# Kernel optimization log

Measured on AMD Instinct MI355X. Metric: run time of the kernel, lower is better.

The kernel has to match this reference:

```python
import jax, jax.numpy as jnp
import numpy as np

D_MODEL = 2048
N_HEADS = 16
D_K = D_MODEL // N_HEADS
D_FF = 5504
THETA = 10000.0
EPS = 1e-5


def rmsnorm(x, g):
    xf = x.astype(jnp.float32)
    ms = jnp.mean(xf * xf, axis=-1, keepdims=True)
    return (xf / jnp.sqrt(ms + EPS) * g).astype(x.dtype)


def rope_tables(seq_len):
    k = jnp.arange(D_K // 2, dtype=jnp.float32)
    freqs = THETA ** (-2.0 * k / float(D_K))          # [d_k/2]
    pos = jnp.arange(seq_len, dtype=jnp.float32)
    phases = pos[:, None] * freqs[None, :]            # [S, d_k/2]
    return jnp.cos(phases), jnp.sin(phases)


def apply_rope(x, cos, sin):
    # x: [..., S, d_k]; cos/sin: [S, d_k/2]
    x_even = x[..., 0::2]
    x_odd = x[..., 1::2]
    e = x_even * cos - x_odd * sin
    o = x_even * sin + x_odd * cos
    out = jnp.stack([e, o], axis=-1)                  # [..., S, d_k/2, 2]
    return out.reshape(x.shape)


def setup_inputs() -> dict:
    key = jax.random.key(0)
    ks = jax.random.split(key, 9)
    def tn(k, shape, fan_in, fan_out):
        std = np.sqrt(2.0 / (fan_in + fan_out))
        return (jax.random.truncated_normal(k, -3.0, 3.0, shape, jnp.float32) * std)
    B, S = 2, 2048
    return {
        "x": jax.random.normal(ks[0], (B, S, D_MODEL), jnp.float32),
        "Wq": tn(ks[1], (D_MODEL, D_MODEL), D_MODEL, D_MODEL),
        "Wk": tn(ks[2], (D_MODEL, D_MODEL), D_MODEL, D_MODEL),
        "Wv": tn(ks[3], (D_MODEL, D_MODEL), D_MODEL, D_MODEL),
        "Wo": tn(ks[4], (D_MODEL, D_MODEL), D_MODEL, D_MODEL),
        "W1": tn(ks[5], (D_FF, D_MODEL), D_MODEL, D_FF),
        "W2": tn(ks[6], (D_MODEL, D_FF), D_FF, D_MODEL),
        "W3": tn(ks[7], (D_FF, D_MODEL), D_MODEL, D_FF),
        "g1": jnp.ones((D_MODEL,), jnp.float32),
        "g2": jnp.ones((D_MODEL,), jnp.float32),
    }


def reference(x, Wq, Wk, Wv, Wo, W1, W2, W3, g1, g2):
    B, S, D = x.shape
    # --- attention sublayer (pre-norm) ---
    xn = rmsnorm(x, g1)
    q = jnp.einsum('bsd,ed->bse', xn, Wq).reshape(B, S, N_HEADS, D_K).transpose(0, 2, 1, 3)
    k = jnp.einsum('bsd,ed->bse', xn, Wk).reshape(B, S, N_HEADS, D_K).transpose(0, 2, 1, 3)
    v = jnp.einsum('bsd,ed->bse', xn, Wv).reshape(B, S, N_HEADS, D_K).transpose(0, 2, 1, 3)
    cos, sin = rope_tables(S)
    q = apply_rope(q, cos, sin)
    k = apply_rope(k, cos, sin)
    scores = jnp.einsum('bhqd,bhkd->bhqk', q, k) / jnp.sqrt(jnp.float32(D_K))
    causal = jnp.tril(jnp.ones((S, S), bool))         # True = keep
    scores = jnp.where(causal, scores, -jnp.inf)
    attn = jax.nn.softmax(scores, axis=-1)
    out = jnp.einsum('bhqk,bhkd->bhqd', attn, v)
    out = out.transpose(0, 2, 1, 3).reshape(B, S, D)
    out = jnp.einsum('bse,de->bsd', out, Wo)
    x_res = x + out
    # --- SwiGLU FFN sublayer (pre-norm) ---
    xn2 = rmsnorm(x_res, g2)
    w1x = jnp.einsum('bsd,fd->bsf', xn2, W1)
    w3x = jnp.einsum('bsd,fd->bsf', xn2, W3)
    h = (w1x * jax.nn.sigmoid(w1x)) * w3x
    ff = jnp.einsum('bsf,df->bsd', h, W2)
    return x_res + ff
```

## Files before the change

### kernel.cpp

```cpp
#include <hip/hip_runtime.h>
#include <hip/hip_bf16.h>
#include <math.h>


typedef __bf16 bf16x8 __attribute__((ext_vector_type(8)));
typedef float f32x4 __attribute__((ext_vector_type(4)));

#define MFMA16(a, b, c) __builtin_amdgcn_mfma_f32_16x16x32_bf16(a, b, c, 0, 0, 0)

__device__ __forceinline__ void async_cp16(const void* g, void* l) {
  __builtin_amdgcn_global_load_lds((__attribute__((address_space(1))) void*)g,
                                   (__attribute__((address_space(3))) void*)l,
                                   16, 0, 0);
}

__global__ __launch_bounds__(256) void cvt_k(const float* __restrict__ s,
                                             __bf16* __restrict__ d, long n) {
  const long i = ((long)blockIdx.x * 256 + threadIdx.x) * 8;
  if (i >= n) return;
  f32x4 a = *(const f32x4*)(s + i);
  f32x4 b = *(const f32x4*)(s + i + 4);
  bf16x8 o;
#pragma unroll
  for (int j = 0; j < 4; ++j) {
    o[j] = (__bf16)a[j];
    o[4 + j] = (__bf16)b[j];
  }
  *(bf16x8*)(d + i) = o;
}

template <int EPI, typename CT, typename RT>
__global__ __launch_bounds__(256) void gemm_bt(
    const __bf16* __restrict__ A, const __bf16* __restrict__ B,
    CT* C, const RT* R, int M, int N, int K) {
  __shared__ __attribute__((aligned(16))) __bf16 sA[128 * 32];
  __shared__ __attribute__((aligned(16))) __bf16 sB[128 * 32];
  const int tid = threadIdx.x;
  const int lane = tid & 63;
  const int wave = tid >> 6;
  const int wm = (wave >> 1) << 6;
  const int wn = (wave & 1) << 6;
  const int ln15 = lane & 15;
  const int kq8 = (lane >> 4) << 3;
  const long blockM = (long)blockIdx.y << 7;
  const long blockN = (long)blockIdx.x << 7;

  const int srow = tid >> 2;
  const int scol = (tid & 3) << 3;
  const __bf16* gA = A + (blockM + srow) * (long)K + scol;
  const __bf16* gB = B + (blockN + srow) * (long)K + scol;
  __bf16* lA = sA + tid * 8;
  __bf16* lB = sB + tid * 8;

  f32x4 acc[4][4] = {};
  const int KT = K >> 5;

  async_cp16(gA, lA);
  async_cp16(gA + 64 * (long)K, lA + 2048);
  async_cp16(gB, lB);
  async_cp16(gB + 64 * (long)K, lB + 2048);

  for (int kt = 0; kt < KT; ++kt) {
    __builtin_amdgcn_s_waitcnt(0);
    __syncthreads();
    bf16x8 af[4], bfr[4];
#pragma unroll
    for (int i = 0; i < 4; ++i)
      af[i] = *(const bf16x8*)&sA[(wm + i * 16 + ln15) * 32 + kq8];
#pragma unroll
    for (int j = 0; j < 4; ++j)
      bfr[j] = *(const bf16x8*)&sB[(wn + j * 16 + ln15) * 32 + kq8];
    __syncthreads();
    if (kt + 1 < KT) {
      const __bf16* a2 = gA + (long)(kt + 1) * 32;
      const __bf16* b2 = gB + (long)(kt + 1) * 32;
      async_cp16(a2, lA);
      async_cp16(a2 + 64 * (long)K, lA + 2048);
      async_cp16(b2, lB);
      async_cp16(b2 + 64 * (long)K, lB + 2048);
    }
#pragma unroll
    for (int i = 0; i < 4; ++i)
#pragma unroll
      for (int j = 0; j < 4; ++j)
        acc[i][j] = MFMA16(af[i], bfr[j], acc[i][j]);
  }

  const int rq4 = (lane >> 4) << 2;
#pragma unroll
  for (int i = 0; i < 4; ++i)
#pragma unroll
    for (int j = 0; j < 4; ++j)
#pragma unroll
      for (int r = 0; r < 4; ++r) {
        const long grow = blockM + wm + i * 16 + rq4 + r;
        const long gcol = blockN + wn + j * 16 + ln15;
        const long idx = grow * N + gcol;
        float v = acc[i][j][r];
        if (EPI == 1) v += (float)R[idx];
        if (EPI == 2) {
          const float w = (float)R[idx];
          v *= w / (1.f + __expf(-w));
        }
        C[idx] = (CT)v;
      }
}

__global__ __launch_bounds__(64) void attn_k(
    const __bf16* __restrict__ q, const __bf16* __restrict__ k,
    const __bf16* __restrict__ v, __bf16* __restrict__ o) {
  __shared__ __attribute__((aligned(16))) __bf16 sP[16 * 32];
  const int lane = threadIdx.x;
  const int ln15 = lane & 15;
  const int quad = lane >> 4;
  const int qt = blockIdx.x;
  const int h = blockIdx.y;
  const int b = blockIdx.z;
  const int S = 2048;
  const int qb = qt << 4;
  const long bh = (long)b * S * 2048 + h * 128;
  const float NEG = -1.0e4f;

  bf16x8 qf[4];
  const __bf16* qp = q + bh + (long)(qb + ln15) * 2048 + quad * 8;
#pragma unroll
  for (int kb = 0; kb < 4; ++kb) qf[kb] = *(const bf16x8*)(qp + kb * 32);

  f32x4 oacc[8] = {};
  float mrow[4] = {NEG, NEG, NEG, NEG};
  float lrow[4] = {};
  const float scale = 0.08838834764831845f;

  const int nkt = (qt + 2) >> 1;
  for (int kt = 0; kt < nkt; ++kt) {
    const int kbase = kt << 5;
    f32x4 s[2] = {};
#pragma unroll
    for (int c = 0; c < 2; ++c) {
      const __bf16* kp = k + bh + (long)(kbase + c * 16 + ln15) * 2048 + quad * 8;
#pragma unroll
      for (int kb = 0; kb < 4; ++kb) {
        bf16x8 kf = *(const bf16x8*)(kp + kb * 32);
        s[c] = MFMA16(qf[kb], kf, s[c]);
      }
    }
#pragma unroll
    for (int r = 0; r < 4; ++r) {
      const int qrow = qb + quad * 4 + r;
      const bool m0 = (kbase + ln15 > qrow);
      const bool m1 = (kbase + 16 + ln15 > qrow);
      const float s0 = m0 ? NEG : s[0][r] * scale;
      const float s1 = m1 ? NEG : s[1][r] * scale;
      float tm = fmaxf(s0, s1);
#pragma unroll
      for (int off = 1; off < 16; off <<= 1) tm = fmaxf(tm, __shfl_xor(tm, off));
      const float mnew = fmaxf(mrow[r], tm);
      const float alpha = __expf(mrow[r] - mnew);
      mrow[r] = mnew;
      const float p0 = m0 ? 0.f : __expf(s0 - mnew);
      const float p1 = m1 ? 0.f : __expf(s1 - mnew);
      float rs = p0 + p1;
#pragma unroll
      for (int off = 1; off < 16; off <<= 1) rs += __shfl_xor(rs, off);
      lrow[r] = lrow[r] * alpha + rs;
#pragma unroll
      for (int nt = 0; nt < 8; ++nt) oacc[nt][r] *= alpha;
      sP[(quad * 4 + r) * 32 + ln15] = (__bf16)p0;
      sP[(quad * 4 + r) * 32 + 16 + ln15] = (__bf16)p1;
    }
    __syncthreads();
    bf16x8 pa = *(const bf16x8*)&sP[ln15 * 32 + quad * 8];
    __syncthreads();
    const __bf16* vbase = v + bh + (long)kbase * 2048;
#pragma unroll
    for (int nt = 0; nt < 8; ++nt) {
      bf16x8 vf;
      const __bf16* vp = vbase + (long)(quad * 8) * 2048 + nt * 16 + ln15;
#pragma unroll
      for (int j = 0; j < 8; ++j) vf[j] = vp[(long)j * 2048];
      oacc[nt] = MFMA16(pa, vf, oacc[nt]);
    }
  }

  __bf16* op = o + bh + (long)qb * 2048;
#pragma unroll
  for (int nt = 0; nt < 8; ++nt)
#pragma unroll
    for (int r = 0; r < 4; ++r)
      op[(long)(quad * 4 + r) * 2048 + nt * 16 + ln15] =
          (__bf16)(oacc[nt][r] / lrow[r]);
}

__global__ __launch_bounds__(256) void rmsnorm_k(
    const float* __restrict__ x, const float* __restrict__ g,
    __bf16* __restrict__ out) {
  __shared__ float red[4];
  const int row = blockIdx.x;
  const int tid = threadIdx.x;
  f32x4 xa = *(const f32x4*)(x + (long)row * 2048 + tid * 8);
  f32x4 xb = *(const f32x4*)(x + (long)row * 2048 + tid * 8 + 4);
  float xf[8];
  float ss = 0.f;
#pragma unroll
  for (int j = 0; j < 4; ++j) {
    xf[j] = xa[j];
    xf[4 + j] = xb[j];
  }
#pragma unroll
  for (int j = 0; j < 8; ++j) ss += xf[j] * xf[j];
#pragma unroll
  for (int off = 32; off > 0; off >>= 1) ss += __shfl_xor(ss, off);
  if ((tid & 63) == 0) red[tid >> 6] = ss;
  __syncthreads();
  const float inv = rsqrtf((red[0] + red[1] + red[2] + red[3]) * (1.f / 2048.f) + 1e-5f);
  f32x4 ga = *(const f32x4*)(g + tid * 8);
  f32x4 gb = *(const f32x4*)(g + tid * 8 + 4);
  bf16x8 ov;
#pragma unroll
  for (int j = 0; j < 4; ++j) {
    ov[j] = (__bf16)(xf[j] * inv * ga[j]);
    ov[4 + j] = (__bf16)(xf[4 + j] * inv * gb[j]);
  }
  *(bf16x8*)(out + (long)row * 2048 + tid * 8) = ov;
}

__global__ __launch_bounds__(256) void rope_k(__bf16* __restrict__ t) {
  const long idx = (long)blockIdx.x * 256 + threadIdx.x;
  const int kp = idx & 63;
  const int h = (idx >> 6) & 15;
  const long row = idx >> 10;
  const int pos = (int)(row & 2047);
  const float freq = exp2f((float)kp * (-13.287712379549449f / 64.0f));
  float sn, cs;
  sincosf((float)pos * freq, &sn, &cs);
  __bf16* p = t + row * 2048 + h * 128 + kp * 2;
  const float e = (float)p[0], od = (float)p[1];
  p[0] = (__bf16)(e * cs - od * sn);
  p[1] = (__bf16)(e * sn + od * cs);
}

extern "C" void kernel_launch(void* const* d_in, const int* in_sizes, int n_in,
                              void* d_out, int out_size, void* d_ws, size_t ws_size,
                              hipStream_t stream) {
  const float* x = (const float*)d_in[0];
  const float* Wq = (const float*)d_in[1];
  const float* Wk = (const float*)d_in[2];
  const float* Wv = (const float*)d_in[3];
  const float* Wo = (const float*)d_in[4];
  const float* W1 = (const float*)d_in[5];
  const float* W2 = (const float*)d_in[6];
  const float* W3 = (const float*)d_in[7];
  const float* g1 = (const float*)d_in[8];
  const float* g2 = (const float*)d_in[9];
  float* out = (float*)d_out;
  char* ws = (char*)d_ws;

  const long NDD = 2048L * 2048;
  const long NFD = 5504L * 2048;
  const long WSLOT = 22544384;
  const long MB16 = 16777216;

  __bf16* wslot = (__bf16*)(ws);
  __bf16* xn = (__bf16*)(ws + WSLOT);
  __bf16* qb = (__bf16*)(ws + WSLOT + MB16);
  __bf16* kb = (__bf16*)(ws + WSLOT + 2 * MB16);
  __bf16* vb = (__bf16*)(ws + WSLOT + 3 * MB16);
  __bf16* attn = xn;
  __bf16* xn2 = vb;
  __bf16* w1x = xn;

  rmsnorm_k<<<4096, 256, 0, stream>>>(x, g1, xn);

  cvt_k<<<2048, 256, 0, stream>>>(Wq, wslot, NDD);
  gemm_bt<0, __bf16, float><<<dim3(16, 32), 256, 0, stream>>>(
      xn, wslot, qb, nullptr, 4096, 2048, 2048);
  cvt_k<<<2048, 256, 0, stream>>>(Wk, wslot, NDD);
  gemm_bt<0, __bf16, float><<<dim3(16, 32), 256, 0, stream>>>(
      xn, wslot, kb, nullptr, 4096, 2048, 2048);
  cvt_k<<<2048, 256, 0, stream>>>(Wv, wslot, NDD);
  gemm_bt<0, __bf16, float><<<dim3(16, 32), 256, 0, stream>>>(
      xn, wslot, vb, nullptr, 4096, 2048, 2048);

  rope_k<<<16384, 256, 0, stream>>>(qb);
  rope_k<<<16384, 256, 0, stream>>>(kb);
  attn_k<<<dim3(128, 16, 2), 64, 0, stream>>>(qb, kb, vb, attn);

  cvt_k<<<2048, 256, 0, stream>>>(Wo, wslot, NDD);
  gemm_bt<1, float, float><<<dim3(16, 32), 256, 0, stream>>>(
      attn, wslot, out, x, 4096, 2048, 2048);

  rmsnorm_k<<<4096, 256, 0, stream>>>(out, g2, xn2);

  cvt_k<<<5504, 256, 0, stream>>>(W1, wslot, NFD);
  gemm_bt<0, __bf16, float><<<dim3(43, 32), 256, 0, stream>>>(
      xn2, wslot, w1x, nullptr, 4096, 5504, 2048);
  cvt_k<<<5504, 256, 0, stream>>>(W3, wslot, NFD);
  gemm_bt<2, __bf16, __bf16><<<dim3(43, 32), 256, 0, stream>>>(
      xn2, wslot, w1x, w1x, 4096, 5504, 2048);
  cvt_k<<<5504, 256, 0, stream>>>(W2, wslot, NFD);
  gemm_bt<1, float, float><<<dim3(16, 32), 256, 0, stream>>>(
      w1x, wslot, out, out, 4096, 2048, 5504);
}
```

Measured before the change: 1.130 ms.

## Pre-transpose V for vectorized attention loads and schedule longest query tiles first

Adds a transpose kernel that writes V as [b, channel, seq] into the weight scratch slot. This lets the attention kernel load each MFMA B-fragment with a single 16-byte vector load instead of eight strided scalar 2-byte loads. It also reverses the query-tile order so the causally longest blocks launch first, which should balance the tail. The cost is one extra kernel and an 8 MB round trip through memory for V.

Result: slower. 1.281 ms (+13.4%).

```diff
diff --git a/kernel.cpp b/kernel.cpp
--- a/kernel.cpp
+++ b/kernel.cpp
@@ -106,19 +106,39 @@
       }
 }
 
+__global__ __launch_bounds__(256) void vt_k(const __bf16* __restrict__ v,
+                                            __bf16* __restrict__ vt) {
+  __shared__ __bf16 sT[64 * 40];
+  const int t = threadIdx.x;
+  const int s0 = blockIdx.x << 5;
+  const int c0 = blockIdx.y << 6;
+  const long b = blockIdx.z;
+  const int sl = t >> 3;
+  const int cg = (t & 7) << 3;
+  bf16x8 val = *(const bf16x8*)(v + (b * 2048 + s0 + sl) * 2048L + c0 + cg);
+#pragma unroll
+  for (int j = 0; j < 8; ++j) sT[(cg + j) * 40 + sl] = val[j];
+  __syncthreads();
+  const int cl = t >> 2;
+  const int sg = (t & 3) << 3;
+  bf16x8 o = *(const bf16x8*)&sT[cl * 40 + sg];
+  *(bf16x8*)(vt + (b * 2048 + c0 + cl) * 2048L + s0 + sg) = o;
+}
+
 __global__ __launch_bounds__(64) void attn_k(
     const __bf16* __restrict__ q, const __bf16* __restrict__ k,
-    const __bf16* __restrict__ v, __bf16* __restrict__ o) {
+    const __bf16* __restrict__ vt, __bf16* __restrict__ o) {
   __shared__ __attribute__((aligned(16))) __bf16 sP[16 * 32];
   const int lane = threadIdx.x;
   const int ln15 = lane & 15;
   const int quad = lane >> 4;
-  const int qt = blockIdx.x;
+  const int qt = (int)gridDim.x - 1 - (int)blockIdx.x;
   const int h = blockIdx.y;
   const int b = blockIdx.z;
   const int S = 2048;
   const int qb = qt << 4;
   const long bh = (long)b * S * 2048 + h * 128;
+  const __bf16* vtp = vt + ((long)b * 2048 + h * 128) * 2048;
   const float NEG = -1.0e4f;
 
   bf16x8 qf[4];
@@ -171,13 +191,10 @@
     __syncthreads();
     bf16x8 pa = *(const bf16x8*)&sP[ln15 * 32 + quad * 8];
     __syncthreads();
-    const __bf16* vbase = v + bh + (long)kbase * 2048;
 #pragma unroll
     for (int nt = 0; nt < 8; ++nt) {
-      bf16x8 vf;
-      const __bf16* vp = vbase + (long)(quad * 8) * 2048 + nt * 16 + ln15;
-#pragma unroll
-      for (int j = 0; j < 8; ++j) vf[j] = vp[(long)j * 2048];
+      bf16x8 vf = *(const bf16x8*)(vtp + (long)(nt * 16 + ln15) * 2048 +
+                                   kbase + quad * 8);
       oacc[nt] = MFMA16(pa, vf, oacc[nt]);
     }
   }
@@ -266,6 +283,7 @@
   __bf16* kb = (__bf16*)(ws + WSLOT + 2 * MB16);
   __bf16* vb = (__bf16*)(ws + WSLOT + 3 * MB16);
   __bf16* attn = xn;
+  __bf16* vtb = wslot;
   __bf16* xn2 = vb;
   __bf16* w1x = xn;
 
@@ -281,9 +299,10 @@
   gemm_bt<0, __bf16, float><<<dim3(16, 32), 256, 0, stream>>>(
       xn, wslot, vb, nullptr, 4096, 2048, 2048);
 
+  vt_k<<<dim3(64, 32, 2), 256, 0, stream>>>(vb, vtb);
   rope_k<<<16384, 256, 0, stream>>>(qb);
   rope_k<<<16384, 256, 0, stream>>>(kb);
-  attn_k<<<dim3(128, 16, 2), 64, 0, stream>>>(qb, kb, vb, attn);
+  attn_k<<<dim3(128, 16, 2), 64, 0, stream>>>(qb, kb, vtb, attn);
 
   cvt_k<<<2048, 256, 0, stream>>>(Wo, wslot, NDD);
   gemm_bt<1, float, float><<<dim3(16, 32), 256, 0, stream>>>(
```

## Pair complementary causal query tiles per attention block and remap blocks to XCDs

Applied to the files above, without the earlier changes.

Each attention workgroup now handles two 16-row query tiles, p and 127-p, so the causal work per block is balanced. K and V fragments loaded from global memory are shared by both tiles' MFMAs, which halves K/V traffic per query row. Blocks are remapped so each XCD handles contiguous (batch, head) panels, which should improve L2 locality. In exchange, register pressure rises (two sets of accumulators, with launch bounds set to 2 waves) and the grid drops to half as many blocks.

Result: faster. 1.028 ms (-9.0%).

```diff
diff --git a/kernel.cpp b/kernel.cpp
--- a/kernel.cpp
+++ b/kernel.cpp
@@ -106,89 +106,149 @@
       }
 }
 
-__global__ __launch_bounds__(64) void attn_k(
+__device__ __forceinline__ void sm_update(const f32x4 s[2], float mrow[4],
+                                          float lrow[4], f32x4 oacc[8],
+                                          __bf16* sP, int qb, int kbase,
+                                          int ln15, int quad) {
+  const float scale = 0.08838834764831845f;
+  const float NEG = -1.0e4f;
+#pragma unroll
+  for (int r = 0; r < 4; ++r) {
+    const int qrow = qb + quad * 4 + r;
+    const bool m0 = (kbase + ln15 > qrow);
+    const bool m1 = (kbase + 16 + ln15 > qrow);
+    const float s0 = m0 ? NEG : s[0][r] * scale;
+    const float s1 = m1 ? NEG : s[1][r] * scale;
+    float tm = fmaxf(s0, s1);
+#pragma unroll
+    for (int off = 1; off < 16; off <<= 1) tm = fmaxf(tm, __shfl_xor(tm, off));
+    const float mnew = fmaxf(mrow[r], tm);
+    const float alpha = __expf(mrow[r] - mnew);
+    mrow[r] = mnew;
+    const float p0 = m0 ? 0.f : __expf(s0 - mnew);
+    const float p1 = m1 ? 0.f : __expf(s1 - mnew);
+    float rs = p0 + p1;
+#pragma unroll
+    for (int off = 1; off < 16; off <<= 1) rs += __shfl_xor(rs, off);
+    lrow[r] = lrow[r] * alpha + rs;
+#pragma unroll
+    for (int nt = 0; nt < 8; ++nt) oacc[nt][r] *= alpha;
+    sP[(quad * 4 + r) * 32 + ln15] = (__bf16)p0;
+    sP[(quad * 4 + r) * 32 + 16 + ln15] = (__bf16)p1;
+  }
+}
+
+__global__ __launch_bounds__(64, 2) void attn_k(
     const __bf16* __restrict__ q, const __bf16* __restrict__ k,
     const __bf16* __restrict__ v, __bf16* __restrict__ o) {
-  __shared__ __attribute__((aligned(16))) __bf16 sP[16 * 32];
+  __shared__ __attribute__((aligned(16))) __bf16 sPA[16 * 32];
+  __shared__ __attribute__((aligned(16))) __bf16 sPB[16 * 32];
   const int lane = threadIdx.x;
   const int ln15 = lane & 15;
   const int quad = lane >> 4;
-  const int qt = blockIdx.x;
-  const int h = blockIdx.y;
-  const int b = blockIdx.z;
+  const int lin = blockIdx.x + 64 * (blockIdx.y + 16 * blockIdx.z);
+  const int xcd = lin & 7;
+  const int j = lin >> 3;
+  const int panel = xcd * 4 + (j >> 6);
+  const int p = j & 63;
+  const int b = panel >> 4;
+  const int h = panel & 15;
   const int S = 2048;
-  const int qb = qt << 4;
+  const int qbA = p << 4;
+  const int qbB = (127 - p) << 4;
   const long bh = (long)b * S * 2048 + h * 128;
+
+  bf16x8 qfA[4], qfB[4];
+  {
+    const __bf16* qpA = q + bh + (long)(qbA + ln15) * 2048 + quad * 8;
+    const __bf16* qpB = q + bh + (long)(qbB + ln15) * 2048 + quad * 8;
+#pragma unroll
+    for (int kb = 0; kb < 4; ++kb) {
+      qfA[kb] = *(const bf16x8*)(qpA + kb * 32);
+      qfB[kb] = *(const bf16x8*)(qpB + kb * 32);
+    }
+  }
+
   const float NEG = -1.0e4f;
-
-  bf16x8 qf[4];
-  const __bf16* qp = q + bh + (long)(qb + ln15) * 2048 + quad * 8;
-#pragma unroll
-  for (int kb = 0; kb < 4; ++kb) qf[kb] = *(const bf16x8*)(qp + kb * 32);
-
-  f32x4 oacc[8] = {};
-  float mrow[4] = {NEG, NEG, NEG, NEG};
-  float lrow[4] = {};
-  const float scale = 0.08838834764831845f;
-
-  const int nkt = (qt + 2) >> 1;
-  for (int kt = 0; kt < nkt; ++kt) {
+  f32x4 oaccA[8] = {}, oaccB[8] = {};
+  float mrowA[4] = {NEG, NEG, NEG, NEG}, mrowB[4] = {NEG, NEG, NEG, NEG};
+  float lrowA[4] = {}, lrowB[4] = {};
+
+  const int nktA = ((p) + 2) >> 1;
+  const int nktB = ((127 - p) + 2) >> 1;
+
+  for (int kt = 0; kt < nktB; ++kt) {
     const int kbase = kt << 5;
-    f32x4 s[2] = {};
-#pragma unroll
-    for (int c = 0; c < 2; ++c) {
-      const __bf16* kp = k + bh + (long)(kbase + c * 16 + ln15) * 2048 + quad * 8;
-#pragma unroll
-      for (int kb = 0; kb < 4; ++kb) {
-        bf16x8 kf = *(const bf16x8*)(kp + kb * 32);
-        s[c] = MFMA16(qf[kb], kf, s[c]);
-      }
-    }
+    const bool doA = (kt < nktA);
+    f32x4 sA[2] = {}, sB[2] = {};
+    if (doA) {
+#pragma unroll
+      for (int c = 0; c < 2; ++c) {
+        const __bf16* kp =
+            k + bh + (long)(kbase + c * 16 + ln15) * 2048 + quad * 8;
+#pragma unroll
+        for (int kb = 0; kb < 4; ++kb) {
+          bf16x8 kf = *(const bf16x8*)(kp + kb * 32);
+          sB[c] = MFMA16(qfB[kb], kf, sB[c]);
+          sA[c] = MFMA16(qfA[kb], kf, sA[c]);
+        }
+      }
+    } else {
+#pragma unroll
+      for (int c = 0; c < 2; ++c) {
+        const __bf16* kp =
+            k + bh + (long)(kbase + c * 16 + ln15) * 2048 + quad * 8;
+#pragma unroll
+        for (int kb = 0; kb < 4; ++kb) {
+          bf16x8 kf = *(const bf16x8*)(kp + kb * 32);
+          sB[c] = MFMA16(qfB[kb], kf, sB[c]);
+        }
+      }
+    }
+
+    sm_update(sB, mrowB, lrowB, oaccB, sPB, qbB, kbase, ln15, quad);
+    if (doA) sm_update(sA, mrowA, lrowA, oaccA, sPA, qbA, kbase, ln15, quad);
+
+    __syncthreads();
+    bf16x8 paB = *(const bf16x8*)&sPB[ln15 * 32 + quad * 8];
+    bf16x8 paA = {};
+    if (doA) paA = *(const bf16x8*)&sPA[ln15 * 32 + quad * 8];
+    __syncthreads();
+
+    const __bf16* vbase = v + bh + (long)kbase * 2048;
+    if (doA) {
+#pragma unroll
+      for (int nt = 0; nt < 8; ++nt) {
+        bf16x8 vf;
+        const __bf16* vp = vbase + (long)(quad * 8) * 2048 + nt * 16 + ln15;
+#pragma unroll
+        for (int jj = 0; jj < 8; ++jj) vf[jj] = vp[(long)jj * 2048];
+        oaccB[nt] = MFMA16(paB, vf, oaccB[nt]);
+        oaccA[nt] = MFMA16(paA, vf, oaccA[nt]);
+      }
+    } else {
+#pragma unroll
+      for (int nt = 0; nt < 8; ++nt) {
+        bf16x8 vf;
+        const __bf16* vp = vbase + (long)(quad * 8) * 2048 + nt * 16 + ln15;
+#pragma unroll
+        for (int jj = 0; jj < 8; ++jj) vf[jj] = vp[(long)jj * 2048];
+        oaccB[nt] = MFMA16(paB, vf, oaccB[nt]);
+      }
+    }
+  }
+
+  __bf16* opB = o + bh + (long)qbB * 2048;
+  __bf16* opA = o + bh + (long)qbA * 2048;
+#pragma unroll
+  for (int nt = 0; nt < 8; ++nt)
 #pragma unroll
     for (int r = 0; r < 4; ++r) {
-      const int qrow = qb + quad * 4 + r;
-      const bool m0 = (kbase + ln15 > qrow);
-      const bool m1 = (kbase + 16 + ln15 > qrow);
-      const float s0 = m0 ? NEG : s[0][r] * scale;
-      const float s1 = m1 ? NEG : s[1][r] * scale;
-      float tm = fmaxf(s0, s1);
-#pragma unroll
-      for (int off = 1; off < 16; off <<= 1) tm = fmaxf(tm, __shfl_xor(tm, off));
-      const float mnew = fmaxf(mrow[r], tm);
-      const float alpha = __expf(mrow[r] - mnew);
-      mrow[r] = mnew;
-      const float p0 = m0 ? 0.f : __expf(s0 - mnew);
-      const float p1 = m1 ? 0.f : __expf(s1 - mnew);
-      float rs = p0 + p1;
-#pragma unroll
-      for (int off = 1; off < 16; off <<= 1) rs += __shfl_xor(rs, off);
-      lrow[r] = lrow[r] * alpha + rs;
-#pragma unroll
-      for (int nt = 0; nt < 8; ++nt) oacc[nt][r] *= alpha;
-      sP[(quad * 4 + r) * 32 + ln15] = (__bf16)p0;
-      sP[(quad * 4 + r) * 32 + 16 + ln15] = (__bf16)p1;
-    }
-    __syncthreads();
-    bf16x8 pa = *(const bf16x8*)&sP[ln15 * 32 + quad * 8];
-    __syncthreads();
-    const __bf16* vbase = v + bh + (long)kbase * 2048;
-#pragma unroll
-    for (int nt = 0; nt < 8; ++nt) {
-      bf16x8 vf;
-      const __bf16* vp = vbase + (long)(quad * 8) * 2048 + nt * 16 + ln15;
-#pragma unroll
-      for (int j = 0; j < 8; ++j) vf[j] = vp[(long)j * 2048];
-      oacc[nt] = MFMA16(pa, vf, oacc[nt]);
-    }
-  }
-
-  __bf16* op = o + bh + (long)qb * 2048;
-#pragma unroll
-  for (int nt = 0; nt < 8; ++nt)
-#pragma unroll
-    for (int r = 0; r < 4; ++r)
-      op[(long)(quad * 4 + r) * 2048 + nt * 16 + ln15] =
-          (__bf16)(oacc[nt][r] / lrow[r]);
+      opB[(long)(quad * 4 + r) * 2048 + nt * 16 + ln15] =
+          (__bf16)(oaccB[nt][r] / lrowB[r]);
+      opA[(long)(quad * 4 + r) * 2048 + nt * 16 + ln15] =
+          (__bf16)(oaccA[nt][r] / lrowA[r]);
+    }
 }
 
 __global__ __launch_bounds__(256) void rmsnorm_k(
@@ -283,7 +343,7 @@
 
   rope_k<<<16384, 256, 0, stream>>>(qb);
   rope_k<<<16384, 256, 0, stream>>>(kb);
-  attn_k<<<dim3(128, 16, 2), 64, 0, stream>>>(qb, kb, vb, attn);
+  attn_k<<<dim3(64, 16, 2), 64, 0, stream>>>(qb, kb, vb, attn);
 
   cvt_k<<<2048, 256, 0, stream>>>(Wo, wslot, NDD);
   gemm_bt<1, float, float><<<dim3(16, 32), 256, 0, stream>>>(
```
